# Optimization experiments

Hardware: AMD Instinct MI355X
Metric: run time of the kernel (lower is better)

Reference implementation:

```python
import jax, jax.numpy as jnp
import numpy as np

B, T = 128, 512
V, P, K = 10002, 500, 20
DC, DP, DT = 300, 100, 50
D = DC + DP + DT
H = 256


def setup_inputs() -> dict:
    key = jax.random.key(0)
    ks = jax.random.split(key, 21)
    s = lambda i, shape: jax.random.normal(ks[i], shape, jnp.float32) * 0.05
    return dict(
        x=jax.random.randint(ks[0], (B, T), 0, V),
        y=jax.random.randint(ks[1], (B, T), 0, K),
        pre_tags=jax.random.randint(ks[2], (B, T), 0, K),
        pinyin_tags=jax.random.randint(ks[3], (B, T), 0, P),
        mask=jnp.ones((B, T), bool),
        char_emb=s(4, (V, DC)),
        tag_emb=s(5, (K, DT)),
        pinyin_emb=s(6, (P, DP)),
        w_ih_f=s(7, (4 * H, D)), w_hh_f=s(8, (4 * H, H)), b_ih_f=s(9, (4 * H,)), b_hh_f=s(10, (4 * H,)),
        w_ih_b=s(11, (4 * H, D)), w_hh_b=s(12, (4 * H, H)), b_ih_b=s(13, (4 * H,)), b_hh_b=s(14, (4 * H,)),
        w_out=s(15, (K, 2 * H)), b_out=s(16, (K,)),
        start_trans=s(17, (K,)), end_trans=s(18, (K,)), trans=s(19, (K, K)),
    )


def _lstm_dir(xs, w_ih, w_hh, b_ih, b_hh, reverse):
    # xs: [T,B,D]; precompute input projection for all steps (one big GEMM)
    pre = jnp.einsum('tbd,gd->tbg', xs, w_ih) + b_ih + b_hh  # [T,B,4H]
    bsz = xs.shape[1]

    def step(carry, gx):
        h, c = carry
        g = gx + h @ w_hh.T
        i, f, gg, o = jnp.split(g, 4, axis=-1)  # torch gate order i,f,g,o
        c = jax.nn.sigmoid(f) * c + jax.nn.sigmoid(i) * jnp.tanh(gg)
        h = jax.nn.sigmoid(o) * jnp.tanh(c)
        return (h, c), h

    init = (jnp.zeros((bsz, H), xs.dtype), jnp.zeros((bsz, H), xs.dtype))
    _, hs = jax.lax.scan(step, init, pre, reverse=reverse)
    return hs  # [T,B,H]


def _emissions(x, pre_tags, pinyin_tags, char_emb, tag_emb, pinyin_emb,
               w_ih_f, w_hh_f, b_ih_f, b_hh_f, w_ih_b, w_hh_b, b_ih_b, b_hh_b,
               w_out, b_out):
    emb = jnp.concatenate([char_emb[x], pinyin_emb[pinyin_tags], tag_emb[pre_tags]], axis=2)  # [B,T,D]
    xs = emb.transpose(1, 0, 2)  # [T,B,D]
    hf = _lstm_dir(xs, w_ih_f, w_hh_f, b_ih_f, b_hh_f, reverse=False)
    hb = _lstm_dir(xs, w_ih_b, w_hh_b, b_ih_b, b_hh_b, reverse=True)
    h = jnp.concatenate([hf, hb], axis=-1)  # [T,B,2H]
    return jnp.einsum('tbh,kh->tbk', h, w_out) + b_out  # emissions [T,B,K]


def _crf_nll(em, tags, mask, start, trans, end):
    # em [T,B,K] (time-major), torchcrf forward with reduction='sum'
    tg = tags.T  # [T,B]
    mk = mask.T.astype(em.dtype)  # [T,B]
    # gold-path score
    first = start[tg[0]] + jnp.take_along_axis(em[0], tg[0][:, None], 1)[:, 0]

    def num_step(score, inputs):
        e_t, t_prev, t_cur, m = inputs
        s = trans[t_prev, t_cur] + jnp.take_along_axis(e_t, t_cur[:, None], 1)[:, 0]
        return score + s * m, None

    score, _ = jax.lax.scan(num_step, first, (em[1:], tg[:-1], tg[1:], mk[1:]))
    last_idx = (mask.sum(1) - 1).astype(jnp.int32)
    last_tag = jnp.take_along_axis(tags, last_idx[:, None].astype(tags.dtype), 1)[:, 0]
    score = score + end[last_tag]
    # partition function via forward algorithm
    alpha0 = start[None, :] + em[0]  # [B,K]

    def den_step(alpha, inputs):
        e_t, m = inputs
        nxt = jax.nn.logsumexp(alpha[:, :, None] + trans[None, :, :] + e_t[:, None, :], axis=1)
        return jnp.where(m[:, None] > 0, nxt, alpha), None

    alpha, _ = jax.lax.scan(den_step, alpha0, (em[1:], mk[1:]))
    logZ = jax.nn.logsumexp(alpha + end[None, :], axis=1)
    llh = jnp.sum(score - logZ)
    return -llh  # module returns -crf(...)


def reference(x, y, pre_tags, pinyin_tags, mask, char_emb, tag_emb, pinyin_emb,
              w_ih_f, w_hh_f, b_ih_f, b_hh_f, w_ih_b, w_hh_b, b_ih_b, b_hh_b,
              w_out, b_out, start_trans, end_trans, trans):
    em = _emissions(x, pre_tags, pinyin_tags, char_emb, tag_emb, pinyin_emb,
                    w_ih_f, w_hh_f, b_ih_f, b_hh_f, w_ih_b, w_hh_b, b_ih_b, b_hh_b,
                    w_out, b_out)
    return _crf_nll(em, y, mask, start_trans, trans, end_trans)
```

## Files before the change

### kernel.cpp

```cpp
#include <hip/hip_runtime.h>
#include <hip/hip_bf16.h>

typedef __attribute__((ext_vector_type(8))) short short8;
typedef __attribute__((ext_vector_type(4))) float float4v;

#if __has_builtin(__builtin_amdgcn_sdot4)
#define DOT4(a, b, c) __builtin_amdgcn_sdot4((int)(a), (int)(b), (c), false)
#else
__device__ __forceinline__ int dot4_(int a, int b, int c) {
  c += (int)(signed char)(a) * (int)(signed char)(b);
  c += (int)(signed char)(a >> 8) * (int)(signed char)(b >> 8);
  c += (int)(signed char)(a >> 16) * (int)(signed char)(b >> 16);
  c += (a >> 24) * (b >> 24);
  return c;
}
#define DOT4(a, b, c) dot4_((int)(a), (int)(b), (c))
#endif

__device__ __forceinline__ float sigmoidf_(float x) {
  return __fdividef(1.f, 1.f + __expf(-x));
}
__device__ __forceinline__ float tanhf_(float x) {
  float e = __expf(2.f * x);
  return 1.f - __fdividef(2.f, e + 1.f);
}
__device__ __forceinline__ float bflo(unsigned int v) {
  return __uint_as_float(v << 16);
}
__device__ __forceinline__ float bfhi(unsigned int v) {
  return __uint_as_float(v & 0xffff0000u);
}
__device__ __forceinline__ void barrier_lgkm() {
  asm volatile("s_waitcnt lgkmcnt(0)\n\ts_barrier" ::: "memory");
}

template <int CTRL>
__device__ __forceinline__ int qadd_i(int v) {
  return v + __builtin_amdgcn_update_dpp(0, v, CTRL, 0xF, 0xF, true);
}
#define XOR1 0xB1
#define XOR2 0x4E

__device__ __forceinline__ unsigned int pack4_(float4 v, float inv) {
  int b0 = (int)rintf(v.x * inv), b1 = (int)rintf(v.y * inv);
  int b2 = (int)rintf(v.z * inv), b3 = (int)rintf(v.w * inv);
  return (unsigned int)((b0 & 0xff) | ((b1 & 0xff) << 8) | ((b2 & 0xff) << 16) |
                        ((b3 & 0xff) << 24));
}

__global__ __launch_bounds__(256) void wquant_kernel(
    const float* __restrict__ whh_f, const float* __restrict__ whh_b,
    unsigned int* __restrict__ wq, float* __restrict__ wsc) {
  const int wave_g = blockIdx.x * 4 + (threadIdx.x >> 6);
  const int lane = threadIdx.x & 63;
  const int dir = wave_g >> 10, row = wave_g & 1023;
  const float* __restrict__ src = (dir ? whh_b : whh_f) + (size_t)row * 256;
  float4 v = ((const float4*)src)[lane];
  float mx = fmaxf(fmaxf(fabsf(v.x), fabsf(v.y)), fmaxf(fabsf(v.z), fabsf(v.w)));
#pragma unroll
  for (int k = 32; k >= 1; k >>= 1) mx = fmaxf(mx, __shfl_xor(mx, k, 64));
  float inv = (mx > 0.f) ? __fdividef(127.f, mx) : 0.f;
  wq[(size_t)wave_g * 64 + lane] = pack4_(v, inv);
  if (lane == 0) wsc[wave_g] = (mx > 0.f) ? (mx / (127.f * 127.f)) : 0.f;
}

__global__ __launch_bounds__(256) void proj_gemm(
    const float* __restrict__ A, int rowsA, int Kdim, int col_off,
    const float* __restrict__ wf, const float* __restrict__ wb,
    const float* __restrict__ bf1, const float* __restrict__ bf2,
    const float* __restrict__ bb1, const float* __restrict__ bb2,
    __hip_bfloat16* __restrict__ out, int add_bias) {
  __shared__ __align__(16) __hip_bfloat16 As[128][40];
  __shared__ __align__(16) __hip_bfloat16 Bs[256][40];
  const int tid = threadIdx.x;
  const int m0 = blockIdx.x * 128, n0 = blockIdx.y * 256;
  const int lane = tid & 63, wave = tid >> 6;
  const int quad = lane >> 4, lm = lane & 15;
  float4v acc[2][16] = {};
  const int ksteps = (Kdim + 31) >> 5;
  const int r2 = tid >> 1, cbase = (tid & 1) << 4;
  const int rb = tid >> 4, cb = (tid & 15) * 2;
  for (int ks = 0; ks < ksteps; ++ks) {
    const int k0 = ks << 5;
#pragma unroll
    for (int e2 = 0; e2 < 8; ++e2) {
      int kk = k0 + cbase + 2 * e2;
      float b0 = 0.f, b1 = 0.f;
      if (m0 + r2 < rowsA && kk < Kdim) {
        float2 v = *(const float2*)(A + (size_t)(m0 + r2) * Kdim + kk);
        b0 = v.x;
        b1 = v.y;
      }
      As[r2][cbase + 2 * e2] = __float2bfloat16(b0);
      As[r2][cbase + 2 * e2 + 1] = __float2bfloat16(b1);
    }
#pragma unroll
    for (int j = 0; j < 16; ++j) {
      int n = n0 + rb + 16 * j;
      const float* __restrict__ wrow =
          (n < 1024) ? (wf + n * 450 + col_off) : (wb + (n - 1024) * 450 + col_off);
      int kk = k0 + cb;
      float b0 = 0.f, b1 = 0.f;
      if (kk < Kdim) {
        float2 v = *(const float2*)(wrow + kk);
        b0 = v.x;
        b1 = v.y;
      }
      Bs[rb + 16 * j][cb] = __float2bfloat16(b0);
      Bs[rb + 16 * j][cb + 1] = __float2bfloat16(b1);
    }
    __syncthreads();
    short8 af0 = *(const short8*)(&As[wave * 32 + lm][quad * 8]);
    short8 af1 = *(const short8*)(&As[wave * 32 + 16 + lm][quad * 8]);
#pragma unroll
    for (int t = 0; t < 16; ++t) {
      short8 bf = *(const short8*)(&Bs[t * 16 + lm][quad * 8]);
      acc[0][t] = __builtin_amdgcn_mfma_f32_16x16x32_bf16(af0, bf, acc[0][t], 0, 0, 0);
      acc[1][t] = __builtin_amdgcn_mfma_f32_16x16x32_bf16(af1, bf, acc[1][t], 0, 0, 0);
    }
    __syncthreads();
  }
#pragma unroll
  for (int mg = 0; mg < 2; ++mg) {
#pragma unroll
    for (int t = 0; t < 16; ++t) {
#pragma unroll
      for (int rr = 0; rr < 4; ++rr) {
        int m = m0 + wave * 32 + mg * 16 + quad * 4 + rr;
        int col = n0 + t * 16 + lm;
        if (m < rowsA) {
          float v = acc[mg][t][rr];
          if (add_bias)
            v += (col < 1024) ? (bf1[col] + bf2[col]) : (bb1[col - 1024] + bb2[col - 1024]);
          int dir = col >> 10, rq = col & 1023;
          int gate = rq >> 8, u = rq & 255;
          out[m * 2048 + dir * 1024 + u * 4 + gate] = __float2bfloat16(v);
        }
      }
    }
  }
}

__global__ __launch_bounds__(256) void lstm_kernel(
    const unsigned int* __restrict__ wq, const float* __restrict__ wsc,
    const int* __restrict__ x, const int* __restrict__ ptags, const int* __restrict__ gtags,
    const char* __restrict__ char_proj, const char* __restrict__ pin_proj,
    const char* __restrict__ tag_proj, __hip_bfloat16* __restrict__ h_out) {
  extern __shared__ __align__(16) char smem[];
  uint4* wlds = (uint4*)smem;
  __hip_bfloat16* hist = (__hip_bfloat16*)(smem + 65536);
  signed char* hb = (signed char*)(smem + 81920);

  const int tid = threadIdx.x;
  const int q = tid >> 2, e = tid & 3;
  const int chain = blockIdx.x;
  const int dir = chain >> 7;
  const int b = chain & 127;
  const int boff = b * 512;

  if (tid < 32) ((int4*)hb)[tid] = make_int4(0, 0, 0, 0);

  int rslot = tid;
  asm volatile("" : "+v"(rslot));

  const unsigned int* __restrict__ wqd = wq + (size_t)dir * 65536;
  const float* __restrict__ wscd = wsc + dir * 1024;
  unsigned int Wreg[12][16];
  float sc4[4];
#pragma unroll
  for (int rr = 0; rr < 16; ++rr) {
    const int grow = (rr & 3) * 256 + 4 * q + (rr >> 2);
    const uint4* __restrict__ srcp = (const uint4*)(wqd + grow * 64 + e * 16);
    if ((rr >> 2) == e) sc4[rr & 3] = wscd[grow];
    if (rr < 12) {
      wlds[tid] = srcp[0];
      wlds[256 + tid] = srcp[1];
      wlds[512 + tid] = srcp[2];
      wlds[768 + tid] = srcp[3];
      uint4 a = wlds[rslot];
      uint4 b4 = wlds[256 + rslot];
      uint4 c4 = wlds[512 + rslot];
      uint4 d4 = wlds[768 + rslot];
      Wreg[rr][0] = a.x;  Wreg[rr][1] = a.y;  Wreg[rr][2] = a.z;  Wreg[rr][3] = a.w;
      Wreg[rr][4] = b4.x; Wreg[rr][5] = b4.y; Wreg[rr][6] = b4.z; Wreg[rr][7] = b4.w;
      Wreg[rr][8] = c4.x; Wreg[rr][9] = c4.y; Wreg[rr][10] = c4.z; Wreg[rr][11] = c4.w;
      Wreg[rr][12] = d4.x; Wreg[rr][13] = d4.y; Wreg[rr][14] = d4.z; Wreg[rr][15] = d4.w;
    } else {
#pragma unroll
      for (int c = 0; c < 4; ++c) wlds[((rr - 12) * 4 + c) * 256 + tid] = srcp[c];
    }
  }
  {
    float* fl = (float*)hist;
#pragma unroll
    for (int g = 0; g < 4; ++g) {
      fl[tid] = sc4[g];
      sc4[g] = fl[rslot];
    }
  }
  __syncthreads();

  const int myu = tid;
  const int pre_off = dir * 2048 + myu * 8;
  float cst = 0.f;
  const uint4* wbase = wlds + tid;

  int t_cur = dir ? 511 : 0;
  int t_nxt = dir ? 510 : 1;
  int xc = x[boff + t_cur], pc_i = ptags[boff + t_cur], gc_i = gtags[boff + t_cur];
  uint2 vc = *(const uint2*)(char_proj + (size_t)xc * 4096 + pre_off);
  uint2 vp = *(const uint2*)(pin_proj + (size_t)pc_i * 4096 + pre_off);
  uint2 vg = *(const uint2*)(tag_proj + (size_t)gc_i * 4096 + pre_off);
  int xn = x[boff + t_nxt], pn = ptags[boff + t_nxt], gn = gtags[boff + t_nxt];

  for (int s = 0; s < 512; ++s) {
    const int t = t_cur;
    const uint2 cv = vc, pv = vp, gv = vg;
    const int t_fut = dir ? (t_nxt > 0 ? t_nxt - 1 : 0) : (t_nxt < 511 ? t_nxt + 1 : 511);
    vc = *(const uint2*)(char_proj + (size_t)xn * 4096 + pre_off);
    vp = *(const uint2*)(pin_proj + (size_t)pn * 4096 + pre_off);
    vg = *(const uint2*)(tag_proj + (size_t)gn * 4096 + pre_off);
    xn = x[boff + t_fut];
    pn = ptags[boff + t_fut];
    gn = gtags[boff + t_fut];

    const signed char* hbase = hb + (s & 1) * 256 + e * 64;
    int acc[16] = {0, 0, 0, 0, 0, 0, 0, 0, 0, 0, 0, 0, 0, 0, 0, 0};
#pragma unroll
    for (int c = 0; c < 4; ++c) {
      uint4 H = *(const uint4*)(hbase + c * 16);
#pragma unroll
      for (int rr = 0; rr < 12; ++rr) {
        acc[rr] = DOT4(Wreg[rr][4 * c + 0], H.x, acc[rr]);
        acc[rr] = DOT4(Wreg[rr][4 * c + 1], H.y, acc[rr]);
        acc[rr] = DOT4(Wreg[rr][4 * c + 2], H.z, acc[rr]);
        acc[rr] = DOT4(Wreg[rr][4 * c + 3], H.w, acc[rr]);
      }
#pragma unroll
      for (int p = 0; p < 4; ++p) {
        uint4 wv = wbase[(p * 4 + c) * 256];
        acc[12 + p] = DOT4(wv.x, H.x, acc[12 + p]);
        acc[12 + p] = DOT4(wv.y, H.y, acc[12 + p]);
        acc[12 + p] = DOT4(wv.z, H.z, acc[12 + p]);
        acc[12 + p] = DOT4(wv.w, H.w, acc[12 + p]);
      }
    }
#pragma unroll
    for (int rr = 0; rr < 16; ++rr) {
      int v = qadd_i<XOR1>(acc[rr]);
      acc[rr] = qadd_i<XOR2>(v);
    }
    int ai = e == 0 ? acc[0] : (e == 1 ? acc[4] : (e == 2 ? acc[8] : acc[12]));
    int af = e == 0 ? acc[1] : (e == 1 ? acc[5] : (e == 2 ? acc[9] : acc[13]));
    int ag = e == 0 ? acc[2] : (e == 1 ? acc[6] : (e == 2 ? acc[10] : acc[14]));
    int ao = e == 0 ? acc[3] : (e == 1 ? acc[7] : (e == 2 ? acc[11] : acc[15]));
    float gi = bflo(cv.x) + bflo(pv.x) + bflo(gv.x) + (float)ai * sc4[0];
    float gf = bfhi(cv.x) + bfhi(pv.x) + bfhi(gv.x) + (float)af * sc4[1];
    float gg = bflo(cv.y) + bflo(pv.y) + bflo(gv.y) + (float)ag * sc4[2];
    float go = bfhi(cv.y) + bfhi(pv.y) + bfhi(gv.y) + (float)ao * sc4[3];
    cst = sigmoidf_(gf) * cst + sigmoidf_(gi) * tanhf_(gg);
    float hval = sigmoidf_(go) * tanhf_(cst);
    hb[((s + 1) & 1) * 256 + myu] = (signed char)(int)rintf(hval * 127.f);
    hist[(s & 31) * 256 + myu] = __float2bfloat16(hval);
    barrier_lgkm();
    if ((s & 15) == 15) {
      const int slotBase = (s & 31) & ~15;
      const int sBase = s - 15;
#pragma unroll
      for (int i = 0; i < 2; ++i) {
        int c = i * 256 + tid;
        int row = c >> 5;
        int col16 = c & 31;
        uint4 v = *(const uint4*)((const char*)hist + (slotBase + row) * 512 + col16 * 16);
        int step_r = sBase + row;
        int t_r = dir ? (511 - step_r) : step_r;
        *(uint4*)((char*)h_out + ((size_t)(chain * 512 + t_r) * 256) * 2 + col16 * 16) = v;
      }
    }
    t_cur = t_nxt;
    t_nxt = t_fut;
  }
}

__global__ __launch_bounds__(256) void emis_kernel(
    const __hip_bfloat16* __restrict__ h_glob, const float* __restrict__ w_out,
    const float* __restrict__ b_out, float* __restrict__ em) {
  __shared__ __align__(16) __hip_bfloat16 As[64][40];
  __shared__ __align__(16) __hip_bfloat16 Bs[32][40];
  const int tid = threadIdx.x;
  const int n0 = blockIdx.x * 64;
  const int lane = tid & 63, wave = tid >> 6, quad = lane >> 4, lm = lane & 15;
  float4v acc[2] = {};
  const int r = tid >> 2, c0 = (tid & 3) << 3;
  const int rb = tid >> 3, cb = (tid & 7) << 2;
  for (int ks = 0; ks < 16; ++ks) {
    const int j0 = ks * 32;
    const int dirk = j0 >> 8, jin = j0 & 255;
    const int n = n0 + r, bb = n >> 9, tt = n & 511;
    const uint4* src =
        (const uint4*)(h_glob + ((size_t)(dirk * 128 + bb) * 512 + tt) * 256 + jin + c0);
    *(uint4*)(&As[r][c0]) = *src;
#pragma unroll
    for (int e = 0; e < 4; ++e) {
      float v = (rb < 20) ? w_out[rb * 512 + j0 + cb + e] : 0.f;
      Bs[rb][cb + e] = __float2bfloat16(v);
    }
    __syncthreads();
    short8 af = *(const short8*)(&As[wave * 16 + lm][quad * 8]);
#pragma unroll
    for (int t2 = 0; t2 < 2; ++t2) {
      short8 bf = *(const short8*)(&Bs[t2 * 16 + lm][quad * 8]);
      acc[t2] = __builtin_amdgcn_mfma_f32_16x16x32_bf16(af, bf, acc[t2], 0, 0, 0);
    }
    __syncthreads();
  }
#pragma unroll
  for (int t2 = 0; t2 < 2; ++t2) {
#pragma unroll
    for (int rr = 0; rr < 4; ++rr) {
      int col = t2 * 16 + lm;
      if (col < 20) {
        int n = n0 + wave * 16 + quad * 4 + rr;
        em[(size_t)n * 20 + col] = acc[t2][rr] + b_out[col];
      }
    }
  }
}

__global__ __launch_bounds__(64) void crf_kernel(
    const float* __restrict__ em, const int* __restrict__ y,
    const float* __restrict__ start_trans, const float* __restrict__ end_trans,
    const float* __restrict__ trans, float* __restrict__ partials) {
  const int b = blockIdx.x;
  const int lane = threadIdx.x;
  const int jj = lane < 20 ? lane : 19;
  const bool act = lane < 20;
  const float* __restrict__ emb = em + (size_t)b * 512 * 20;
  const int* __restrict__ yb = y + b * 512;

  float s_part = 0.f;
#pragma unroll
  for (int i = 0; i < 8; ++i) {
    int t = lane + 64 * i;
    int yc = yb[t];
    float v = emb[t * 20 + yc];
    v += (t == 0) ? start_trans[yc] : trans[yb[t - 1] * 20 + yc];
    s_part += v;
  }
#pragma unroll
  for (int k = 32; k >= 1; k >>= 1) s_part += __shfl_xor(s_part, k, 64);
  float score = s_part + end_trans[yb[511]];

  float ET[20];
#pragma unroll
  for (int i = 0; i < 20; ++i) ET[i] = __expf(trans[i * 20 + jj]);
  float alpha = act ? (start_trans[jj] + emb[jj]) : -1e30f;
  float P = alpha;
#pragma unroll
  for (int k = 32; k >= 1; k >>= 1) P = fmaxf(P, __shfl_xor(P, k, 64));

  float eC = emb[1 * 20 + jj];
  float eN = emb[2 * 20 + jj];
  for (int t = 1; t < 512; ++t) {
    if ((t & 15) == 0) {
      P = alpha;
#pragma unroll
      for (int k = 32; k >= 1; k >>= 1) P = fmaxf(P, __shfl_xor(P, k, 64));
    }
    float ex = __expf(alpha - P);
    float s0 = 0.f, s1 = 0.f;
#pragma unroll
    for (int i = 0; i < 20; i += 2) {
      float e0 = __int_as_float(__builtin_amdgcn_readlane(__float_as_int(ex), i));
      float e1 = __int_as_float(__builtin_amdgcn_readlane(__float_as_int(ex), i + 1));
      s0 = fmaf(e0, ET[i], s0);
      s1 = fmaf(e1, ET[i + 1], s1);
    }
    int tf = t + 2 < 512 ? t + 2 : 511;
    float eF = emb[tf * 20 + jj];
    if (act) alpha = P + __logf(s0 + s1) + eC;
    eC = eN;
    eN = eF;
  }
  float v = act ? (alpha + end_trans[jj]) : -1e30f;
  float Pz = v;
#pragma unroll
  for (int k = 32; k >= 1; k >>= 1) Pz = fmaxf(Pz, __shfl_xor(Pz, k, 64));
  float e2 = __expf(v - Pz);
#pragma unroll
  for (int k = 32; k >= 1; k >>= 1) e2 += __shfl_xor(e2, k, 64);
  float logZ = Pz + __logf(e2);
  if (lane == 0) partials[b] = logZ - score;
}

__global__ __launch_bounds__(128) void reduce_kernel(const float* __restrict__ partials,
                                                     float* __restrict__ out) {
  const int tid = threadIdx.x;
  float v = partials[tid];
#pragma unroll
  for (int k = 32; k >= 1; k >>= 1) v += __shfl_xor(v, k, 64);
  __shared__ float tmp[2];
  if ((tid & 63) == 0) tmp[tid >> 6] = v;
  __syncthreads();
  if (tid == 0) out[0] = tmp[0] + tmp[1];
}

extern "C" void kernel_launch(void* const* d_in, const int* in_sizes, int n_in,
                              void* d_out, int out_size, void* d_ws, size_t ws_size,
                              hipStream_t stream) {
  const int* x = (const int*)d_in[0];
  const int* y = (const int*)d_in[1];
  const int* pre_tags = (const int*)d_in[2];
  const int* pinyin_tags = (const int*)d_in[3];
  const float* char_emb = (const float*)d_in[5];
  const float* tag_emb = (const float*)d_in[6];
  const float* pinyin_emb = (const float*)d_in[7];
  const float* w_ih_f = (const float*)d_in[8];
  const float* w_hh_f = (const float*)d_in[9];
  const float* b_ih_f = (const float*)d_in[10];
  const float* b_hh_f = (const float*)d_in[11];
  const float* w_ih_b = (const float*)d_in[12];
  const float* w_hh_b = (const float*)d_in[13];
  const float* b_ih_b = (const float*)d_in[14];
  const float* b_hh_b = (const float*)d_in[15];
  const float* w_out = (const float*)d_in[16];
  const float* b_out = (const float*)d_in[17];
  const float* start_trans = (const float*)d_in[18];
  const float* end_trans = (const float*)d_in[19];
  const float* trans = (const float*)d_in[20];

  char* ws = (char*)d_ws;
  __hip_bfloat16* char_proj = (__hip_bfloat16*)(ws);
  __hip_bfloat16* pin_proj = (__hip_bfloat16*)(ws + 40968192);
  __hip_bfloat16* tag_proj = (__hip_bfloat16*)(ws + 43016192);
  __hip_bfloat16* h_glob = (__hip_bfloat16*)(ws + 43098112);
  float* em = (float*)(ws + 110206976);
  float* partials = (float*)(ws + 115449856);
  unsigned int* wq = (unsigned int*)(ws + 110206976);
  float* wsc = (float*)(ws + 110206976 + 524288);

  wquant_kernel<<<512, 256, 0, stream>>>(w_hh_f, w_hh_b, wq, wsc);

  proj_gemm<<<dim3(79, 8), 256, 0, stream>>>(char_emb, 10002, 300, 0, w_ih_f, w_ih_b,
                                             nullptr, nullptr, nullptr, nullptr, char_proj, 0);
  proj_gemm<<<dim3(4, 8), 256, 0, stream>>>(pinyin_emb, 500, 100, 300, w_ih_f, w_ih_b,
                                            nullptr, nullptr, nullptr, nullptr, pin_proj, 0);
  proj_gemm<<<dim3(1, 8), 256, 0, stream>>>(tag_emb, 20, 50, 400, w_ih_f, w_ih_b,
                                            b_ih_f, b_hh_f, b_ih_b, b_hh_b, tag_proj, 1);

  const int lstm_lds = 82432;
  hipFuncSetAttribute((const void*)lstm_kernel, hipFuncAttributeMaxDynamicSharedMemorySize,
                      lstm_lds);
  lstm_kernel<<<256, 256, lstm_lds, stream>>>(wq, wsc, x, pinyin_tags, pre_tags,
                                              (const char*)char_proj, (const char*)pin_proj,
                                              (const char*)tag_proj, h_glob);

  emis_kernel<<<1024, 256, 0, stream>>>(h_glob, w_out, b_out, em);
  crf_kernel<<<128, 64, 0, stream>>>(em, y, start_trans, end_trans, trans, partials);
  reduce_kernel<<<1, 128, 0, stream>>>(partials, (float*)d_out);
}
```

Before: 1.056 ms.

## Split LSTM recurrence across 512 threads with all weights in registers

The LSTM block grows from 256 to 512 threads so each thread holds 8 weight rows in registers instead of 12 in registers plus 4 streamed from LDS each step. This removes the per-step LDS weight reads and shrinks LDS from about 82 KB to about 17 KB. Two threads now compute each hidden unit's gates, only half write h, and the history flush uses one pass. The cost is more waves per block taking part in each per-step barrier, plus duplicated gate math.

```diff
diff --git a/kernel.cpp b/kernel.cpp
--- a/kernel.cpp
+++ b/kernel.cpp
@@ -141,15 +141,14 @@
   }
 }
 
-__global__ __launch_bounds__(256) void lstm_kernel(
+__global__ __launch_bounds__(512, 2) void lstm_kernel(
     const unsigned int* __restrict__ wq, const float* __restrict__ wsc,
     const int* __restrict__ x, const int* __restrict__ ptags, const int* __restrict__ gtags,
     const char* __restrict__ char_proj, const char* __restrict__ pin_proj,
     const char* __restrict__ tag_proj, __hip_bfloat16* __restrict__ h_out) {
   extern __shared__ __align__(16) char smem[];
-  uint4* wlds = (uint4*)smem;
-  __hip_bfloat16* hist = (__hip_bfloat16*)(smem + 65536);
-  signed char* hb = (signed char*)(smem + 81920);
+  __hip_bfloat16* hist = (__hip_bfloat16*)smem;
+  signed char* hb = (signed char*)(smem + 16384);
 
   const int tid = threadIdx.x;
   const int q = tid >> 2, e = tid & 3;
@@ -165,45 +164,41 @@
 
   const unsigned int* __restrict__ wqd = wq + (size_t)dir * 65536;
   const float* __restrict__ wscd = wsc + dir * 1024;
-  unsigned int Wreg[12][16];
+  const int sub_e = e & 1;
+  const int u_mine = 2 * q + sub_e;
+
+  unsigned int Wreg[8][16];
+  {
+    uint4* lbuf = (uint4*)smem;
+#pragma unroll
+    for (int rr = 0; rr < 8; ++rr) {
+      const int g = rr & 3, sub = rr >> 2;
+      const int grow = g * 256 + 2 * q + sub;
+      const uint4* __restrict__ srcp = (const uint4*)(wqd + grow * 64 + e * 16);
+#pragma unroll
+      for (int c = 0; c < 4; ++c) {
+        lbuf[tid] = srcp[c];
+        uint4 a = lbuf[rslot];
+        Wreg[rr][4 * c + 0] = a.x;
+        Wreg[rr][4 * c + 1] = a.y;
+        Wreg[rr][4 * c + 2] = a.z;
+        Wreg[rr][4 * c + 3] = a.w;
+      }
+    }
+  }
   float sc4[4];
-#pragma unroll
-  for (int rr = 0; rr < 16; ++rr) {
-    const int grow = (rr & 3) * 256 + 4 * q + (rr >> 2);
-    const uint4* __restrict__ srcp = (const uint4*)(wqd + grow * 64 + e * 16);
-    if ((rr >> 2) == e) sc4[rr & 3] = wscd[grow];
-    if (rr < 12) {
-      wlds[tid] = srcp[0];
-      wlds[256 + tid] = srcp[1];
-      wlds[512 + tid] = srcp[2];
-      wlds[768 + tid] = srcp[3];
-      uint4 a = wlds[rslot];
-      uint4 b4 = wlds[256 + rslot];
-      uint4 c4 = wlds[512 + rslot];
-      uint4 d4 = wlds[768 + rslot];
-      Wreg[rr][0] = a.x;  Wreg[rr][1] = a.y;  Wreg[rr][2] = a.z;  Wreg[rr][3] = a.w;
-      Wreg[rr][4] = b4.x; Wreg[rr][5] = b4.y; Wreg[rr][6] = b4.z; Wreg[rr][7] = b4.w;
-      Wreg[rr][8] = c4.x; Wreg[rr][9] = c4.y; Wreg[rr][10] = c4.z; Wreg[rr][11] = c4.w;
-      Wreg[rr][12] = d4.x; Wreg[rr][13] = d4.y; Wreg[rr][14] = d4.z; Wreg[rr][15] = d4.w;
-    } else {
-#pragma unroll
-      for (int c = 0; c < 4; ++c) wlds[((rr - 12) * 4 + c) * 256 + tid] = srcp[c];
-    }
-  }
   {
-    float* fl = (float*)hist;
+    float* fl = (float*)(smem + 8192);
 #pragma unroll
     for (int g = 0; g < 4; ++g) {
-      fl[tid] = sc4[g];
+      fl[tid] = wscd[g * 256 + u_mine];
       sc4[g] = fl[rslot];
     }
   }
   __syncthreads();
 
-  const int myu = tid;
-  const int pre_off = dir * 2048 + myu * 8;
+  const int pre_off = dir * 2048 + u_mine * 8;
   float cst = 0.f;
-  const uint4* wbase = wlds + tid;
 
   int t_cur = dir ? 511 : 0;
   int t_nxt = dir ? 510 : 1;
@@ -214,7 +209,6 @@
   int xn = x[boff + t_nxt], pn = ptags[boff + t_nxt], gn = gtags[boff + t_nxt];
 
   for (int s = 0; s < 512; ++s) {
-    const int t = t_cur;
     const uint2 cv = vc, pv = vp, gv = vg;
     const int t_fut = dir ? (t_nxt > 0 ? t_nxt - 1 : 0) : (t_nxt < 511 ? t_nxt + 1 : 511);
     vc = *(const uint2*)(char_proj + (size_t)xn * 4096 + pre_off);
@@ -225,57 +219,47 @@
     gn = gtags[boff + t_fut];
 
     const signed char* hbase = hb + (s & 1) * 256 + e * 64;
-    int acc[16] = {0, 0, 0, 0, 0, 0, 0, 0, 0, 0, 0, 0, 0, 0, 0, 0};
+    int acc[8] = {0, 0, 0, 0, 0, 0, 0, 0};
 #pragma unroll
     for (int c = 0; c < 4; ++c) {
       uint4 H = *(const uint4*)(hbase + c * 16);
 #pragma unroll
-      for (int rr = 0; rr < 12; ++rr) {
+      for (int rr = 0; rr < 8; ++rr) {
         acc[rr] = DOT4(Wreg[rr][4 * c + 0], H.x, acc[rr]);
         acc[rr] = DOT4(Wreg[rr][4 * c + 1], H.y, acc[rr]);
         acc[rr] = DOT4(Wreg[rr][4 * c + 2], H.z, acc[rr]);
         acc[rr] = DOT4(Wreg[rr][4 * c + 3], H.w, acc[rr]);
       }
-#pragma unroll
-      for (int p = 0; p < 4; ++p) {
-        uint4 wv = wbase[(p * 4 + c) * 256];
-        acc[12 + p] = DOT4(wv.x, H.x, acc[12 + p]);
-        acc[12 + p] = DOT4(wv.y, H.y, acc[12 + p]);
-        acc[12 + p] = DOT4(wv.z, H.z, acc[12 + p]);
-        acc[12 + p] = DOT4(wv.w, H.w, acc[12 + p]);
-      }
-    }
-#pragma unroll
-    for (int rr = 0; rr < 16; ++rr) {
+    }
+#pragma unroll
+    for (int rr = 0; rr < 8; ++rr) {
       int v = qadd_i<XOR1>(acc[rr]);
       acc[rr] = qadd_i<XOR2>(v);
     }
-    int ai = e == 0 ? acc[0] : (e == 1 ? acc[4] : (e == 2 ? acc[8] : acc[12]));
-    int af = e == 0 ? acc[1] : (e == 1 ? acc[5] : (e == 2 ? acc[9] : acc[13]));
-    int ag = e == 0 ? acc[2] : (e == 1 ? acc[6] : (e == 2 ? acc[10] : acc[14]));
-    int ao = e == 0 ? acc[3] : (e == 1 ? acc[7] : (e == 2 ? acc[11] : acc[15]));
+    int ai = sub_e ? acc[4] : acc[0];
+    int af = sub_e ? acc[5] : acc[1];
+    int ag = sub_e ? acc[6] : acc[2];
+    int ao = sub_e ? acc[7] : acc[3];
     float gi = bflo(cv.x) + bflo(pv.x) + bflo(gv.x) + (float)ai * sc4[0];
     float gf = bfhi(cv.x) + bfhi(pv.x) + bfhi(gv.x) + (float)af * sc4[1];
     float gg = bflo(cv.y) + bflo(pv.y) + bflo(gv.y) + (float)ag * sc4[2];
     float go = bfhi(cv.y) + bfhi(pv.y) + bfhi(gv.y) + (float)ao * sc4[3];
     cst = sigmoidf_(gf) * cst + sigmoidf_(gi) * tanhf_(gg);
     float hval = sigmoidf_(go) * tanhf_(cst);
-    hb[((s + 1) & 1) * 256 + myu] = (signed char)(int)rintf(hval * 127.f);
-    hist[(s & 31) * 256 + myu] = __float2bfloat16(hval);
+    if (e < 2) {
+      hb[((s + 1) & 1) * 256 + u_mine] = (signed char)(int)rintf(hval * 127.f);
+      hist[(s & 31) * 256 + u_mine] = __float2bfloat16(hval);
+    }
     barrier_lgkm();
     if ((s & 15) == 15) {
       const int slotBase = (s & 31) & ~15;
       const int sBase = s - 15;
-#pragma unroll
-      for (int i = 0; i < 2; ++i) {
-        int c = i * 256 + tid;
-        int row = c >> 5;
-        int col16 = c & 31;
-        uint4 v = *(const uint4*)((const char*)hist + (slotBase + row) * 512 + col16 * 16);
-        int step_r = sBase + row;
-        int t_r = dir ? (511 - step_r) : step_r;
-        *(uint4*)((char*)h_out + ((size_t)(chain * 512 + t_r) * 256) * 2 + col16 * 16) = v;
-      }
+      const int row = tid >> 5;
+      const int col16 = tid & 31;
+      uint4 v = *(const uint4*)((const char*)hist + (slotBase + row) * 512 + col16 * 16);
+      int step_r = sBase + row;
+      int t_r = dir ? (511 - step_r) : step_r;
+      *(uint4*)((char*)h_out + ((size_t)(chain * 512 + t_r) * 256) * 2 + col16 * 16) = v;
     }
     t_cur = t_nxt;
     t_nxt = t_fut;
@@ -448,10 +432,10 @@
   proj_gemm<<<dim3(1, 8), 256, 0, stream>>>(tag_emb, 20, 50, 400, w_ih_f, w_ih_b,
                                             b_ih_f, b_hh_f, b_ih_b, b_hh_b, tag_proj, 1);
 
-  const int lstm_lds = 82432;
+  const int lstm_lds = 16896;
   hipFuncSetAttribute((const void*)lstm_kernel, hipFuncAttributeMaxDynamicSharedMemorySize,
                       lstm_lds);
-  lstm_kernel<<<256, 256, lstm_lds, stream>>>(wq, wsc, x, pinyin_tags, pre_tags,
+  lstm_kernel<<<256, 512, lstm_lds, stream>>>(wq, wsc, x, pinyin_tags, pre_tags,
                                               (const char*)char_proj, (const char*)pin_proj,
                                               (const char*)tag_proj, h_glob);
 
```

New measurement: 1.088 ms. 3.1% more time.
